# Optimization experiments

Hardware: AMD Instinct MI355X
Metric: run time of the kernel (lower is better)

Reference implementation:

```python
import jax, jax.numpy as jnp
import numpy as np


def setup_inputs() -> dict:
    key = jax.random.key(0)
    k1, k2, k3 = jax.random.split(key, 3)
    B, T, D, U = 256, 1024, 128, 256
    x = jax.random.normal(k1, (B, T, D), dtype=jnp.float32)
    h0 = jnp.zeros((B, U), dtype=jnp.float32)
    W = jax.random.normal(k2, (D + U, U), dtype=jnp.float32) * 0.05
    bias = jax.random.normal(k3, (U,), dtype=jnp.float32) * 0.05
    return {"x": x, "h0": h0, "W": W, "bias": bias}


def reference(x, h0, W, bias):
    # x: [B, T, D], h0: [B, U], W: [D+U, U], bias: [U]
    # Per step: Ht = tanh(concat([Ht, x_t], -1) @ W + bias)
    U = h0.shape[-1]
    Wh = W[:U]   # [U, U] part multiplying the state (concat order is (Ht, inputs))
    Wx = W[U:]   # [D, U] part multiplying the input
    # Precompute input projections for all timesteps in one big GEMM.
    x_proj = jnp.einsum('btd,du->btu', x, Wx) + bias  # [B, T, U]

    def step(h, xp_t):
        h_new = jnp.tanh(h @ Wh + xp_t)
        return h_new, h_new

    # scan over time: xs must be time-major
    _, hs = jax.lax.scan(step, h0, jnp.swapaxes(x_proj, 0, 1))  # hs: [T, B, U]
    return jnp.swapaxes(hs, 0, 1)  # [B, T, U]
```

## Files before the change

kernel.cpp:

```cpp
#include <hip/hip_runtime.h>


typedef _Float16 half8 __attribute__((ext_vector_type(8)));
typedef _Float16 half4v __attribute__((ext_vector_type(4)));
typedef float floatx4 __attribute__((ext_vector_type(4)));

constexpr int B = 256, T = 1024, D = 128, U = 256;
constexpr int NSL = (U + D) / 32;
constexpr int QS  = 16 * 16 + 16;
constexpr int SS  = 4 * QS;
constexpr int BUF = NSL * SS;

__device__ __forceinline__ float fexp2(float v) {
#if __has_builtin(__builtin_amdgcn_exp2f)
    return __builtin_amdgcn_exp2f(v);
#else
    return exp2f(v);
#endif
}
__device__ __forceinline__ float frcp(float v) {
#if __has_builtin(__builtin_amdgcn_rcpf)
    return __builtin_amdgcn_rcpf(v);
#else
    return 1.0f / v;
#endif
}
__device__ __forceinline__ float fast_tanh(float v) {
    float e = fexp2(2.8853900817779268f * v);
    return 1.0f - 2.0f * frcp(e + 1.0f);
}

__device__ __forceinline__ void cvt_write8(void* dst, float4 lo, float4 hi) {
    half8 h;
    h[0] = (_Float16)lo.x; h[1] = (_Float16)lo.y;
    h[2] = (_Float16)lo.z; h[3] = (_Float16)lo.w;
    h[4] = (_Float16)hi.x; h[5] = (_Float16)hi.y;
    h[6] = (_Float16)hi.z; h[7] = (_Float16)hi.w;
    *reinterpret_cast<half8*>(dst) = h;
}
__device__ __forceinline__ void cvt_write4(void* dst, float4 v) {
    half4v h;
    h[0] = (_Float16)v.x; h[1] = (_Float16)v.y;
    h[2] = (_Float16)v.z; h[3] = (_Float16)v.w;
    *reinterpret_cast<half4v*>(dst) = h;
}

__global__ __launch_bounds__(512, 2)
void rnn_mfma_kernel(const float* __restrict__ x, const float* __restrict__ h0,
                     const float* __restrict__ W, const float* __restrict__ bias,
                     float* __restrict__ out)
{
    __shared__ __align__(16) unsigned char lds[2 * BUF];

    const int tid  = threadIdx.x;
    const int lane = tid & 63;
    const int wv   = tid >> 6;
    const int l15  = lane & 15;
    const int quad = lane >> 4;
    const int b0   = blockIdx.x * 16;

    half8 wf[2][NSL];
    float bv[2];
#pragma unroll
    for (int nt = 0; nt < 2; ++nt) {
        const int n = 32 * wv + 16 * nt + l15;
        bv[nt] = bias[n];
#pragma unroll
        for (int s = 0; s < NSL; ++s) {
            half8 f;
#pragma unroll
            for (int j = 0; j < 8; ++j) {
                const int k = 32 * s + 8 * quad + j;
            f[j] = (_Float16)W[(size_t)k * U + n];
            }
            wf[nt][s] = f;
        }
    }

    {
        const int sm = tid >> 5;
        const int cc = tid & 31;
        const float* hp = h0 + (size_t)(b0 + sm) * U + 8 * cc;
        cvt_write8(lds + (cc >> 2) * SS + (cc & 3) * QS + sm * 16,
                   *reinterpret_cast<const float4*>(hp),
                   *reinterpret_cast<const float4*>(hp + 4));
    }
    const int sm = tid >> 5;
    const int f4 = tid & 31;
    const int c8 = f4 >> 1;
    const float* xbase = x + (size_t)(b0 + sm) * T * D + 4 * f4;
    const int xslot = (8 + (c8 >> 2)) * SS + (c8 & 3) * QS + sm * 16 + (f4 & 1) * 8;
    cvt_write4(lds + xslot, *reinterpret_cast<const float4*>(xbase));

    float4 p = *reinterpret_cast<const float4*>(xbase + D);

    __syncthreads();

    const int aoff = quad * QS + l15 * 16;

    for (int t = 0; t < T; ++t) {
        const int cur = t & 1, nxt = cur ^ 1;

        const int tp = (t + 2 < T) ? (t + 2) : (T - 1);
        float4 q = *reinterpret_cast<const float4*>(xbase + (size_t)D * tp);

        half8 a[NSL];
        const unsigned char* ab = lds + cur * BUF + aoff;
#pragma unroll
        for (int s = 0; s < NSL; ++s)
            a[s] = *reinterpret_cast<const half8*>(ab + s * SS);

        floatx4 acc[2];
#pragma unroll
        for (int nt = 0; nt < 2; ++nt)
            acc[nt] = (floatx4){bv[nt], bv[nt], bv[nt], bv[nt]};
#pragma unroll
        for (int s = 0; s < NSL; ++s)
#pragma unroll
            for (int nt = 0; nt < 2; ++nt)
                acc[nt] = __builtin_amdgcn_mfma_f32_16x16x32_f16(
                              a[s], wf[nt][s], acc[nt], 0, 0, 0);

        unsigned char* hb = lds + nxt * BUF;
        float* orow = out + (size_t)t * U;
#pragma unroll
        for (int nt = 0; nt < 2; ++nt) {
            const int n = 32 * wv + 16 * nt + l15;
#pragma unroll
            for (int r = 0; r < 4; ++r) {
                const int m = 4 * quad + r;
                const float h = fast_tanh(acc[nt][r]);
                orow[(size_t)(b0 + m) * T * U + n] = h;
                *reinterpret_cast<_Float16*>(
                    hb + (n >> 5) * SS + ((n >> 3) & 3) * QS + m * 16 + (n & 7) * 2)
                    = (_Float16)h;
            }
        }

        cvt_write4(hb + xslot, p);
        p = q;

        __syncthreads();
    }
}

extern "C" void kernel_launch(void* const* d_in, const int* in_sizes, int n_in,
                              void* d_out, int out_size, void* d_ws, size_t ws_size,
                              hipStream_t stream) {
    const float* x    = (const float*)d_in[0];
    const float* h0   = (const float*)d_in[1];
    const float* W    = (const float*)d_in[2];
    const float* bias = (const float*)d_in[3];
    float* out = (float*)d_out;

    hipLaunchKernelGGL(rnn_mfma_kernel, dim3(B / 16), dim3(512), 0, stream,
                       x, h0, W, bias, out);
}
```

Baseline: 1.264 ms.

## Prescale weights for tanh, reorder MFMAs x-first, unroll time by two

Folds the tanh exp2 scale constant into the fp16 weights and bias so the per-step multiply disappears. Each step now issues the input-projection MFMAs before the state MFMAs, raises wave priority around the MFMA block, precomputes output pointers and LDS publish offsets, and unrolls time by two so the double-buffer offsets and the prefetch register swap become compile-time. The aim is to shorten the serial per-step critical path. Scaling the weights before fp16 conversion slightly changes rounding.

Measured after the change: 1.083 ms. 14.4% less time.

```diff
diff --git a/kernel.cpp b/kernel.cpp
--- a/kernel.cpp
+++ b/kernel.cpp
@@ -10,6 +10,8 @@
 constexpr int QS  = 16 * 16 + 16;
 constexpr int SS  = 4 * QS;
 constexpr int BUF = NSL * SS;
+
+constexpr float TANH_K = 2.8853900817779268f;
 
 __device__ __forceinline__ float fexp2(float v) {
 #if __has_builtin(__builtin_amdgcn_exp2f)
@@ -25,8 +27,8 @@
     return 1.0f / v;
 #endif
 }
-__device__ __forceinline__ float fast_tanh(float v) {
-    float e = fexp2(2.8853900817779268f * v);
+__device__ __forceinline__ float tanh_prescaled(float a) {
+    float e = fexp2(a);
     return 1.0f - 2.0f * frcp(e + 1.0f);
 }
 
@@ -64,24 +66,24 @@
 #pragma unroll
     for (int nt = 0; nt < 2; ++nt) {
         const int n = 32 * wv + 16 * nt + l15;
-        bv[nt] = bias[n];
+        bv[nt] = bias[n] * TANH_K;
 #pragma unroll
         for (int s = 0; s < NSL; ++s) {
             half8 f;
 #pragma unroll
             for (int j = 0; j < 8; ++j) {
                 const int k = 32 * s + 8 * quad + j;
-            f[j] = (_Float16)W[(size_t)k * U + n];
+                f[j] = (_Float16)(W[(size_t)k * U + n] * TANH_K);
             }
             wf[nt][s] = f;
         }
     }
 
     {
-        const int sm = tid >> 5;
+        const int hm = tid >> 5;
         const int cc = tid & 31;
-        const float* hp = h0 + (size_t)(b0 + sm) * U + 8 * cc;
-        cvt_write8(lds + (cc >> 2) * SS + (cc & 3) * QS + sm * 16,
+        const float* hp = h0 + (size_t)(b0 + hm) * U + 8 * cc;
+        cvt_write8(lds + (cc >> 2) * SS + (cc & 3) * QS + hm * 16,
                    *reinterpret_cast<const float4*>(hp),
                    *reinterpret_cast<const float4*>(hp + 4));
     }
@@ -93,55 +95,79 @@
     cvt_write4(lds + xslot, *reinterpret_cast<const float4*>(xbase));
 
     float4 p = *reinterpret_cast<const float4*>(xbase + D);
+    float4 q;
 
     __syncthreads();
 
     const int aoff = quad * QS + l15 * 16;
 
-    for (int t = 0; t < T; ++t) {
-        const int cur = t & 1, nxt = cur ^ 1;
+    floatx4 acc0[2];
+#pragma unroll
+    for (int nt = 0; nt < 2; ++nt)
+        acc0[nt] = (floatx4){bv[nt], bv[nt], bv[nt], bv[nt]};
+    float* optr[8];
+    int    pubo[8];
+#pragma unroll
+    for (int i = 0; i < 8; ++i) {
+        const int nt = i >> 2, r = i & 3;
+        const int n = 32 * wv + 16 * nt + l15;
+        const int m = 4 * quad + r;
+        optr[i] = out + (size_t)(b0 + m) * T * U + n;
+        pubo[i] = (n >> 5) * SS + ((n >> 3) & 3) * QS + m * 16 + (n & 7) * 2;
+    }
 
-        const int tp = (t + 2 < T) ? (t + 2) : (T - 1);
-        float4 q = *reinterpret_cast<const float4*>(xbase + (size_t)D * tp);
+#define STEP(tt, CO, NO, PP, QQ)                                               \
+    do {                                                                       \
+        const int t_ = (tt);                                                   \
+        const int tp_ = (t_ + 2 < T) ? (t_ + 2) : (T - 1);                     \
+        QQ = *reinterpret_cast<const float4*>(xbase + (size_t)D * tp_);        \
+        const unsigned char* ab = lds + (CO) + aoff;                           \
+        half8 ax[4];                                                           \
+        _Pragma("unroll")                                                      \
+        for (int s = 0; s < 4; ++s)                                            \
+            ax[s] = *reinterpret_cast<const half8*>(ab + (8 + s) * SS);        \
+        half8 ah[8];                                                           \
+        _Pragma("unroll")                                                      \
+        for (int s = 0; s < 8; ++s)                                            \
+            ah[s] = *reinterpret_cast<const half8*>(ab + s * SS);              \
+        floatx4 acc[2];                                                        \
+        acc[0] = acc0[0]; acc[1] = acc0[1];                                    \
+        __builtin_amdgcn_s_setprio(1);                                         \
+        _Pragma("unroll")                                                      \
+        for (int s = 0; s < 4; ++s)                                            \
+            _Pragma("unroll")                                                  \
+            for (int nt = 0; nt < 2; ++nt)                                     \
+                acc[nt] = __builtin_amdgcn_mfma_f32_16x16x32_f16(              \
+                              ax[s], wf[nt][8 + s], acc[nt], 0, 0, 0);         \
+        _Pragma("unroll")                                                      \
+        for (int s = 0; s < 8; ++s)                                            \
+            _Pragma("unroll")                                                  \
+            for (int nt = 0; nt < 2; ++nt)                                     \
+                acc[nt] = __builtin_amdgcn_mfma_f32_16x16x32_f16(              \
+                              ah[s], wf[nt][s], acc[nt], 0, 0, 0);             \
+        __builtin_amdgcn_s_setprio(0);                                         \
+        float hv[8];                                                           \
+        _Pragma("unroll")                                                      \
+        for (int i = 0; i < 8; ++i)                                            \
+            hv[i] = tanh_prescaled(acc[i >> 2][i & 3]);                        \
+                                     \
+        _Pragma("unroll")                                                      \
+        for (int i = 0; i < 8; ++i)                                            \
+            optr[i][(size_t)t_ * U] = hv[i];                                   \
+                \
+        _Pragma("unroll")                                                      \
+        for (int i = 0; i < 8; ++i)                                            \
+            *reinterpret_cast<_Float16*>(lds + (NO) + pubo[i]) =               \
+                (_Float16)hv[i];                                               \
+        cvt_write4(lds + (NO) + xslot, PP);                                    \
+        __syncthreads();                                                       \
+    } while (0)
 
-        half8 a[NSL];
-        const unsigned char* ab = lds + cur * BUF + aoff;
-#pragma unroll
-        for (int s = 0; s < NSL; ++s)
-            a[s] = *reinterpret_cast<const half8*>(ab + s * SS);
-
-        floatx4 acc[2];
-#pragma unroll
-        for (int nt = 0; nt < 2; ++nt)
-            acc[nt] = (floatx4){bv[nt], bv[nt], bv[nt], bv[nt]};
-#pragma unroll
-        for (int s = 0; s < NSL; ++s)
-#pragma unroll
-            for (int nt = 0; nt < 2; ++nt)
-                acc[nt] = __builtin_amdgcn_mfma_f32_16x16x32_f16(
-                              a[s], wf[nt][s], acc[nt], 0, 0, 0);
-
-        unsigned char* hb = lds + nxt * BUF;
-        float* orow = out + (size_t)t * U;
-#pragma unroll
-        for (int nt = 0; nt < 2; ++nt) {
-            const int n = 32 * wv + 16 * nt + l15;
-#pragma unroll
-            for (int r = 0; r < 4; ++r) {
-                const int m = 4 * quad + r;
-                const float h = fast_tanh(acc[nt][r]);
-                orow[(size_t)(b0 + m) * T * U + n] = h;
-                *reinterpret_cast<_Float16*>(
-                    hb + (n >> 5) * SS + ((n >> 3) & 3) * QS + m * 16 + (n & 7) * 2)
-                    = (_Float16)h;
-            }
-        }
-
-        cvt_write4(hb + xslot, p);
-        p = q;
-
-        __syncthreads();
+    for (int t = 0; t < T; t += 2) {
+        STEP(t,     0,   BUF, p, q);
+        STEP(t + 1, BUF, 0,   q, p);
     }
+#undef STEP
 }
 
 extern "C" void kernel_launch(void* const* d_in, const int* in_sizes, int n_in,
```
